# Performance work log

Measured on AMD Instinct MI355X. Metric: run time of the kernel, lower is better.

Reference implementation:

```python
import jax, jax.numpy as jnp
import numpy as np

N = 50000          # num nodes
E = 1_600_000      # num edges (avg degree 32)
F = 512            # node_dim
C = 64             # num_clusters
O = 256            # output_dim


def setup_inputs() -> dict:
    key = jax.random.key(0)
    ks = jax.random.split(key, 9)
    lim_p = 1.0 / np.sqrt(F)
    inp = {
        "x": jax.random.normal(ks[0], (N, F), dtype=jnp.float32),
        "edge_index": jax.random.randint(ks[1], (2, E), 0, N, dtype=jnp.int64),
        "batch": jnp.zeros((N,), dtype=jnp.int64),
        # gnn_pool: Linear(F, C)
        "Wp": jax.random.uniform(ks[2], (F, C), jnp.float32, -lim_p, lim_p),
        "bp": jax.random.uniform(ks[3], (C,), jnp.float32, -lim_p, lim_p),
        # gnn_embed: Linear(F, F)
        "We": jax.random.uniform(ks[4], (F, F), jnp.float32, -lim_p, lim_p),
        "be": jax.random.uniform(ks[5], (F,), jnp.float32, -lim_p, lim_p),
        # projection: Linear(F, O)
        "Wo": jax.random.uniform(ks[6], (F, O), jnp.float32, -lim_p, lim_p),
        "bo": jax.random.uniform(ks[7], (O,), jnp.float32, -lim_p, lim_p),
    }
    return inp


def reference(x, edge_index, batch, Wp, bp, We, be, Wo, bo):
    # s = softmax(gnn_pool(x), -1): soft cluster assignments  [N, C]
    s = jax.nn.softmax(x @ Wp + bp, axis=-1)
    # h = gnn_embed(x)  [N, F]
    h = x @ We + be
    # dense_diff_pool pooled features: out = s^T h  -> [C, F]
    # (out_adj = s^T A s and the link/entropy reg are computed by the
    #  original but discarded; they do not affect the returned output.)
    pooled = jnp.einsum("nc,nf->cf", s, h)
    # PyG dense_diff_pool unsqueezes 2D inputs to batch dim 1 -> [1, C, F]
    out = pooled[None] @ Wo + bo  # [1, C, O]
    return out
```

## Files before the change

kernel.cpp:

```cpp
#include <hip/hip_runtime.h>
#include <hip/hip_bf16.h>

typedef __attribute__((ext_vector_type(8))) short short8;
typedef __attribute__((ext_vector_type(4))) float floatx4;
typedef __attribute__((ext_vector_type(4))) unsigned uint4v;
typedef __attribute__((ext_vector_type(4))) unsigned short ushort4v;

#define FDIM 512
#define CDIM 64
#define ODIM 256
#define TR   32
#define XSF  516
#define STS 40
#define MAXP 256
#define RSW(r) ((((r) >> 3) & 3) << 2)

__device__ __forceinline__ ushort f2bf(float f) {
    union { float f; unsigned u; } v; v.f = f;
    unsigned r = v.u + 0x7FFFu + ((v.u >> 16) & 1u);
    return (ushort)(r >> 16);
}
__device__ __forceinline__ float bf2f(unsigned hi16) {
    union { unsigned u; float f; } v; v.u = hi16 << 16; return v.f;
}

__device__ __forceinline__ void gld16(const float* g, float* lds_base) {
    __builtin_amdgcn_global_load_lds(
        (const __attribute__((address_space(1))) unsigned int*)(const void*)g,
        (__attribute__((address_space(3))) unsigned int*)(void*)lds_base,
        16, 0, 0);
}

__global__ __launch_bounds__(256) void kWpT(const float* __restrict__ Wp,
                                            ushort* __restrict__ WpT) {
    int g = blockIdx.x * 256 + threadIdx.x;
    int f = g >> 6, c = g & 63;
    WpT[c * FDIM + f] = f2bf(Wp[f * CDIM + c]);
}

__global__ __launch_bounds__(512, 2) void kFused(
        const float* __restrict__ x, const ushort* __restrict__ WpT,
        const float* __restrict__ bp, ushort* __restrict__ part,
        float* __restrict__ cpart, int N, int nTiles, int P) {
    __shared__ float  xsf[2][TR * XSF + 16];
    __shared__ ushort sT[CDIM][STS];
    __shared__ float  red1[TR][4];
    __shared__ float  red2[TR][4];
    __shared__ float  cred[CDIM][2];

    const int t    = threadIdx.x;
    const int w    = t >> 6;
    const int lane = t & 63;
    const int l16  = lane & 15;
    const int q    = lane >> 4;
    const int ci   = w & 3;
    const int rg   = w >> 2;

    floatx4 acc[4][4];
#pragma unroll
    for (int mt = 0; mt < 4; ++mt)
#pragma unroll
        for (int nt = 0; nt < 4; ++nt) acc[mt][nt] = (floatx4){0.f, 0.f, 0.f, 0.f};
    float csp[4] = {0.f, 0.f, 0.f, 0.f};

    float bpv[4];
#pragma unroll
    for (int reg = 0; reg < 4; ++reg) bpv[reg] = bp[16 * ci + 4 * q + reg];

    const ushort* wb = WpT + (size_t)(16 * ci + l16) * FDIM + q * 8;
    short8 af[4][4];
#pragma unroll
    for (int kb = 0; kb < 4; ++kb)
#pragma unroll
        for (int ki = 0; ki < 4; ++ki)
            af[kb][ki] = *(const short8*)(wb + kb * 128 + ki * 32);

    auto stage = [&](int tile, float* xb) {
        const int row0s = tile * TR;
#pragma unroll
        for (int i = 0; i < 8; ++i) {
            const int c0 = w * 8 + i;
            const int r  = c0 >> 1;
            const int h  = c0 & 1;
            float* lb = xb + r * XSF + RSW(r) + h * 256;
            if (row0s + r < N) {
                const float* g = x + (size_t)(row0s + r) * FDIM + h * 256 + lane * 4;
                gld16(g, lb);
            } else {
                *(floatx4*)(lb + lane * 4) = (floatx4){0.f, 0.f, 0.f, 0.f};
            }
        }
    };

    stage(blockIdx.x, xsf[0]);
    __syncthreads();

    int it = 0;
    for (int tile = blockIdx.x; tile < nTiles; tile += P, ++it) {
        float* xb = xsf[it & 1];
        if (tile + P < nTiles) stage(tile + P, xsf[(it & 1) ^ 1]);

        const int row0 = tile * TR;

        floatx4 acc1 = (floatx4){0.f, 0.f, 0.f, 0.f};
        const int prow = 16 * rg + l16;
        const float* xr = xb + prow * XSF + RSW(prow);
#pragma unroll
        for (int kb = 0; kb < 4; ++kb) {
#pragma unroll
            for (int ki = 0; ki < 4; ++ki) {
                const int off = kb * 128 + ki * 32 + q * 8;
                floatx4 u0 = *(const floatx4*)(xr + off);
                floatx4 u1 = *(const floatx4*)(xr + off + 4);
                short8 b;
                b[0] = (short)f2bf(u0[0]); b[1] = (short)f2bf(u0[1]);
                b[2] = (short)f2bf(u0[2]); b[3] = (short)f2bf(u0[3]);
                b[4] = (short)f2bf(u1[0]); b[5] = (short)f2bf(u1[1]);
                b[6] = (short)f2bf(u1[2]); b[7] = (short)f2bf(u1[3]);
                acc1 = __builtin_amdgcn_mfma_f32_16x16x32_bf16(af[kb][ki], b, acc1, 0, 0, 0);
            }
        }

        const int row = prow;
        float lg[4];
#pragma unroll
        for (int reg = 0; reg < 4; ++reg) lg[reg] = acc1[reg] + bpv[reg];
        float m = fmaxf(fmaxf(lg[0], lg[1]), fmaxf(lg[2], lg[3]));
        m = fmaxf(m, __shfl_xor(m, 16));
        m = fmaxf(m, __shfl_xor(m, 32));
        if (lane < 16) red1[16 * rg + lane][ci] = m;
        __syncthreads();
        const float rmax = fmaxf(fmaxf(red1[row][0], red1[row][1]),
                                 fmaxf(red1[row][2], red1[row][3]));
        float p = 0.f;
#pragma unroll
        for (int reg = 0; reg < 4; ++reg) {
            float e = __expf(lg[reg] - rmax);
            lg[reg] = e; p += e;
        }
        p += __shfl_xor(p, 16);
        p += __shfl_xor(p, 32);
        if (lane < 16) red2[16 * rg + lane][ci] = p;
        __syncthreads();
        const float rsi = 1.0f / (red2[row][0] + red2[row][1] +
                                  red2[row][2] + red2[row][3]);
        const bool valid = (row0 + row) < N;
#pragma unroll
        for (int reg = 0; reg < 4; ++reg) {
            float s = valid ? lg[reg] * rsi : 0.f;
            sT[16 * ci + 4 * q + reg][row] = f2bf(s);
            csp[reg] += s;
        }
        __syncthreads();

        short8 as_[4];
#pragma unroll
        for (int mt = 0; mt < 4; ++mt)
            as_[mt] = *(const short8*)&sT[16 * mt + l16][q * 8];
#pragma unroll
        for (int nt = 0; nt < 4; ++nt) {
            const int f = 64 * w + 16 * nt + l16;
            short8 b;
#pragma unroll
            for (int j = 0; j < 8; ++j)
                b[j] = (short)f2bf(xb[(q * 8 + j) * XSF + 4 * q + f]);
#pragma unroll
            for (int mt = 0; mt < 4; ++mt)
                acc[mt][nt] = __builtin_amdgcn_mfma_f32_16x16x32_bf16(
                    as_[mt], b, acc[mt][nt], 0, 0, 0);
        }

        __syncthreads();
    }

#pragma unroll
    for (int reg = 0; reg < 4; ++reg) {
        float v = csp[reg];
        v += __shfl_xor(v, 1); v += __shfl_xor(v, 2);
        v += __shfl_xor(v, 4); v += __shfl_xor(v, 8);
        if (l16 == 0) cred[16 * ci + 4 * q + reg][rg] = v;
    }
    __syncthreads();
    if (t < 64) cpart[(size_t)blockIdx.x * CDIM + t] = cred[t][0] + cred[t][1];

    ushort* xf = (ushort*)xsf;
#pragma unroll
    for (int mt = 0; mt < 4; ++mt)
#pragma unroll
        for (int nt = 0; nt < 4; ++nt)
#pragma unroll
            for (int reg = 0; reg < 4; ++reg)
                xf[(16 * mt + 4 * q + reg) * FDIM + 64 * w + 16 * nt + l16] =
                    f2bf(acc[mt][nt][reg]);
    __syncthreads();
    const uint4v* src = (const uint4v*)xf;
    uint4v* dst = (uint4v*)(part + (size_t)blockIdx.x * (CDIM * FDIM));
#pragma unroll
    for (int i = 0; i < 8; ++i)
        dst[i * 512 + t] = src[i * 512 + t];
}

__global__ __launch_bounds__(512) void kR(const ushort* __restrict__ part,
                                          const float* __restrict__ cpart,
                                          float* __restrict__ colsum,
                                          float* __restrict__ Mp,
                                          int P, int pch) {
    __shared__ float ws8[8];
    const int c = blockIdx.x, pc = blockIdx.y, t = threadIdx.x;
    const int g  = t >> 7;
    const int f0 = (t & 127) << 2;
    const int p0 = pc * pch, p1 = min(p0 + pch, P);

    float s0 = 0.f, s1 = 0.f, s2 = 0.f, s3 = 0.f;
    for (int p = p0 + g; p < p1; p += 4) {
        const ushort4v v = *(const ushort4v*)(part + (size_t)p * (CDIM * FDIM)
                                              + (size_t)c * FDIM + f0);
        s0 += bf2f((unsigned)v[0]); s1 += bf2f((unsigned)v[1]);
        s2 += bf2f((unsigned)v[2]); s3 += bf2f((unsigned)v[3]);
    }
    floatx4 o = (floatx4){s0, s1, s2, s3};
    *(floatx4*)(Mp + (((size_t)(pc * 4 + g) * CDIM + c) * FDIM + f0)) = o;

    float cv = 0.f;
    {
        int p = p0 + t;
        if (p < p1) cv = cpart[(size_t)p * CDIM + c];
    }
    cv += __shfl_xor(cv, 1);  cv += __shfl_xor(cv, 2);
    cv += __shfl_xor(cv, 4);  cv += __shfl_xor(cv, 8);
    cv += __shfl_xor(cv, 16); cv += __shfl_xor(cv, 32);
    if ((t & 63) == 0) ws8[t >> 6] = cv;
    __syncthreads();
    if (t == 0) {
        float tot = 0.f;
#pragma unroll
        for (int i = 0; i < 8; ++i) tot += ws8[i];
        atomicAdd(colsum + c, tot);
    }
}

__global__ __launch_bounds__(512) void kC(const float* __restrict__ Mp,
                                          const float* __restrict__ colsum,
                                          const float* __restrict__ We,
                                          const float* __restrict__ be,
                                          const float* __restrict__ Wo,
                                          const float* __restrict__ bo,
                                          float* __restrict__ out) {
    __shared__ float Mrow[512];
    __shared__ float pooled[512];
    __shared__ float halves[2][256];
    const int c = blockIdx.x, t = threadIdx.x;

    float sum = 0.f;
#pragma unroll
    for (int pc = 0; pc < 32; ++pc)
        sum += Mp[((size_t)pc * CDIM + c) * FDIM + t];
    Mrow[t] = sum;
    __syncthreads();

    float a = colsum[c] * be[t];
#pragma unroll 16
    for (int k = 0; k < FDIM; ++k)
        a = fmaf(Mrow[k], We[(size_t)k * FDIM + t], a);
    pooled[t] = a;
    __syncthreads();

    const int o = t & 255, h = t >> 8;
    float b = 0.f;
#pragma unroll 16
    for (int kk = 0; kk < 256; ++kk) {
        int k = h * 256 + kk;
        b = fmaf(pooled[k], Wo[(size_t)k * ODIM + o], b);
    }
    halves[h][o] = b;
    __syncthreads();
    if (t < 256)
        out[(size_t)c * ODIM + t] = halves[0][t] + halves[1][t] + bo[t];
}

extern "C" void kernel_launch(void* const* d_in, const int* in_sizes, int n_in,
                              void* d_out, int out_size, void* d_ws, size_t ws_size,
                              hipStream_t stream) {
    const float* x  = (const float*)d_in[0];
    const float* Wp = (const float*)d_in[3];
    const float* bp = (const float*)d_in[4];
    const float* We = (const float*)d_in[5];
    const float* be = (const float*)d_in[6];
    const float* Wo = (const float*)d_in[7];
    const float* bo = (const float*)d_in[8];
    float* out = (float*)d_out;

    const int N = in_sizes[0] / FDIM;
    const int nTiles = (N + TR - 1) / TR;

    char*   wsb    = (char*)d_ws;
    ushort* WpT    = (ushort*)wsb;
    float*  colsum = (float*)(wsb + 65536);
    float*  cpart  = (float*)(wsb + 66560);
    float*  Mp     = (float*)(wsb + 266752);
    const size_t PART_OFF = 4461056;
    ushort* part   = (ushort*)(wsb + PART_OFF);

    size_t avail = (ws_size > PART_OFF + 65536) ? (ws_size - PART_OFF) / 65536 : 1;
    int P = (int)(avail < (size_t)MAXP ? avail : (size_t)MAXP);
    if (P > nTiles) P = nTiles;
    if (P < 1) P = 1;
    const int pch = (P + 7) / 8;

    hipMemsetAsync(colsum, 0, 256, stream);
    kWpT<<<128, 256, 0, stream>>>(Wp, WpT);
    kFused<<<P, 512, 0, stream>>>(x, WpT, bp, part, cpart, N, nTiles, P);
    kR<<<dim3(CDIM, 8), 512, 0, stream>>>(part, cpart, colsum, Mp, P, pch);
    kC<<<CDIM, 512, 0, stream>>>(Mp, colsum, We, be, Wo, bo, out);
}
```

Measured before the change: 223.0 us.

## Fold Wp transpose into fused kernel, split MFMA chain, use light barriers

Removes the separate Wp transpose/convert kernel: each thread gathers and converts its Wp fragment directly from fp32 global memory in the fused kernel, which saves one launch. The single logits MFMA accumulator is split into two independent chains to shorten the dependency latency. __syncthreads is replaced by a lgkmcnt wait plus s_barrier inside the tile loop. Launch bounds move from 2 blocks per CU to 1, giving more registers at the cost of occupancy. The strided fp32 Wp gather adds some uncoalesced prologue reads per block.

```diff
diff --git a/kernel.cpp b/kernel.cpp
--- a/kernel.cpp
+++ b/kernel.cpp
@@ -11,7 +11,7 @@
 #define ODIM 256
 #define TR   32
 #define XSF  516
-#define STS 40
+#define STS  40
 #define MAXP 256
 #define RSW(r) ((((r) >> 3) & 3) << 2)
 
@@ -31,15 +31,14 @@
         16, 0, 0);
 }
 
-__global__ __launch_bounds__(256) void kWpT(const float* __restrict__ Wp,
-                                            ushort* __restrict__ WpT) {
-    int g = blockIdx.x * 256 + threadIdx.x;
-    int f = g >> 6, c = g & 63;
-    WpT[c * FDIM + f] = f2bf(Wp[f * CDIM + c]);
-}
-
-__global__ __launch_bounds__(512, 2) void kFused(
-        const float* __restrict__ x, const ushort* __restrict__ WpT,
+#define LBAR() do {                                            \
+    asm volatile("s_waitcnt lgkmcnt(0)" ::: "memory");         \
+    __builtin_amdgcn_s_barrier();                              \
+    asm volatile("" ::: "memory");                             \
+} while (0)
+
+__global__ __launch_bounds__(512, 1) void kFused(
+        const float* __restrict__ x, const float* __restrict__ Wp,
         const float* __restrict__ bp, ushort* __restrict__ part,
         float* __restrict__ cpart, int N, int nTiles, int P) {
     __shared__ float  xsf[2][TR * XSF + 16];
@@ -67,13 +66,21 @@
 #pragma unroll
     for (int reg = 0; reg < 4; ++reg) bpv[reg] = bp[16 * ci + 4 * q + reg];
 
-    const ushort* wb = WpT + (size_t)(16 * ci + l16) * FDIM + q * 8;
     short8 af[4][4];
-#pragma unroll
-    for (int kb = 0; kb < 4; ++kb)
-#pragma unroll
-        for (int ki = 0; ki < 4; ++ki)
-            af[kb][ki] = *(const short8*)(wb + kb * 128 + ki * 32);
+    {
+        const int c = 16 * ci + l16;
+#pragma unroll
+        for (int kb = 0; kb < 4; ++kb)
+#pragma unroll
+            for (int ki = 0; ki < 4; ++ki) {
+                short8 a;
+#pragma unroll
+                for (int j = 0; j < 8; ++j)
+                    a[j] = (short)f2bf(
+                        Wp[(size_t)(kb * 128 + ki * 32 + q * 8 + j) * CDIM + c]);
+                af[kb][ki] = a;
+            }
+    }
 
     auto stage = [&](int tile, float* xb) {
         const int row0s = tile * TR;
@@ -102,11 +109,12 @@
 
         const int row0 = tile * TR;
 
-        floatx4 acc1 = (floatx4){0.f, 0.f, 0.f, 0.f};
+        floatx4 a1a = (floatx4){0.f, 0.f, 0.f, 0.f};
+        floatx4 a1b = (floatx4){0.f, 0.f, 0.f, 0.f};
         const int prow = 16 * rg + l16;
         const float* xr = xb + prow * XSF + RSW(prow);
 #pragma unroll
-        for (int kb = 0; kb < 4; ++kb) {
+        for (int kb = 0; kb < 4; ++kb)
 #pragma unroll
             for (int ki = 0; ki < 4; ++ki) {
                 const int off = kb * 128 + ki * 32 + q * 8;
@@ -117,19 +125,21 @@
                 b[2] = (short)f2bf(u0[2]); b[3] = (short)f2bf(u0[3]);
                 b[4] = (short)f2bf(u1[0]); b[5] = (short)f2bf(u1[1]);
                 b[6] = (short)f2bf(u1[2]); b[7] = (short)f2bf(u1[3]);
-                acc1 = __builtin_amdgcn_mfma_f32_16x16x32_bf16(af[kb][ki], b, acc1, 0, 0, 0);
+                if (kb & 1)
+                    a1b = __builtin_amdgcn_mfma_f32_16x16x32_bf16(af[kb][ki], b, a1b, 0, 0, 0);
+                else
+                    a1a = __builtin_amdgcn_mfma_f32_16x16x32_bf16(af[kb][ki], b, a1a, 0, 0, 0);
             }
-        }
 
         const int row = prow;
         float lg[4];
 #pragma unroll
-        for (int reg = 0; reg < 4; ++reg) lg[reg] = acc1[reg] + bpv[reg];
+        for (int reg = 0; reg < 4; ++reg) lg[reg] = a1a[reg] + a1b[reg] + bpv[reg];
         float m = fmaxf(fmaxf(lg[0], lg[1]), fmaxf(lg[2], lg[3]));
         m = fmaxf(m, __shfl_xor(m, 16));
         m = fmaxf(m, __shfl_xor(m, 32));
         if (lane < 16) red1[16 * rg + lane][ci] = m;
-        __syncthreads();
+        LBAR();
         const float rmax = fmaxf(fmaxf(red1[row][0], red1[row][1]),
                                  fmaxf(red1[row][2], red1[row][3]));
         float p = 0.f;
@@ -141,7 +151,7 @@
         p += __shfl_xor(p, 16);
         p += __shfl_xor(p, 32);
         if (lane < 16) red2[16 * rg + lane][ci] = p;
-        __syncthreads();
+        LBAR();
         const float rsi = 1.0f / (red2[row][0] + red2[row][1] +
                                   red2[row][2] + red2[row][3]);
         const bool valid = (row0 + row) < N;
@@ -151,7 +161,7 @@
             sT[16 * ci + 4 * q + reg][row] = f2bf(s);
             csp[reg] += s;
         }
-        __syncthreads();
+        LBAR();
 
         short8 as_[4];
 #pragma unroll
@@ -183,7 +193,7 @@
     __syncthreads();
     if (t < 64) cpart[(size_t)blockIdx.x * CDIM + t] = cred[t][0] + cred[t][1];
 
-    ushort* xf = (ushort*)xsf;
+    ushort* xf = (ushort*)&xsf[0][0];
 #pragma unroll
     for (int mt = 0; mt < 4; ++mt)
 #pragma unroll
@@ -294,11 +304,10 @@
     const int nTiles = (N + TR - 1) / TR;
 
     char*   wsb    = (char*)d_ws;
-    ushort* WpT    = (ushort*)wsb;
-    float*  colsum = (float*)(wsb + 65536);
-    float*  cpart  = (float*)(wsb + 66560);
-    float*  Mp     = (float*)(wsb + 266752);
-    const size_t PART_OFF = 4461056;
+    float*  colsum = (float*)wsb;
+    float*  cpart  = (float*)(wsb + 1024);
+    float*  Mp     = (float*)(wsb + 66560);
+    const size_t PART_OFF = 4260864;
     ushort* part   = (ushort*)(wsb + PART_OFF);
 
     size_t avail = (ws_size > PART_OFF + 65536) ? (ws_size - PART_OFF) / 65536 : 1;
@@ -308,8 +317,7 @@
     const int pch = (P + 7) / 8;
 
     hipMemsetAsync(colsum, 0, 256, stream);
-    kWpT<<<128, 256, 0, stream>>>(Wp, WpT);
-    kFused<<<P, 512, 0, stream>>>(x, WpT, bp, part, cpart, N, nTiles, P);
+    kFused<<<P, 512, 0, stream>>>(x, Wp, bp, part, cpart, N, nTiles, P);
     kR<<<dim3(CDIM, 8), 512, 0, stream>>>(part, cpart, colsum, Mp, P, pch);
     kC<<<CDIM, 512, 0, stream>>>(Mp, colsum, We, be, Wo, bo, out);
 }
```

After: 220.6 us. About the same (-1.1%).
